# Kernel tuning notes

Hardware: AMD Instinct MI355X
Metric: run time of the kernel (lower is better)

The kernel has to match this reference:

```python
import jax, jax.numpy as jnp
from jax import lax
import numpy as np

B, N, D_MODEL = 4, 2048, 768
D_INNER = 1536      # int(2.0 * d_model)
DT_RANK = 48        # ceil(768 / 16)
EPS = 1e-5


def setup_inputs() -> dict:
    key = jax.random.key(0)
    ks = jax.random.split(key, 9)
    x = jax.random.normal(ks[0], (B, N, D_MODEL), jnp.float32)
    # BFS order: a permutation of node ids
    sorted_index = jax.random.permutation(ks[1], N).astype(jnp.int32)
    # parent BFS position of node at BFS position i, must be < i; root (i=0) has -1
    pos = jnp.arange(N)
    r = jax.random.randint(ks[2], (N,), 0, N)
    sorted_parent = jnp.where(pos == 0, -1, r % jnp.maximum(pos, 1)).astype(jnp.int32)
    s = 0.02
    in_proj_w = jax.random.normal(ks[3], (D_MODEL, 2 * D_INNER), jnp.float32) * s
    x_proj_w = jax.random.normal(ks[4], (D_INNER, DT_RANK + 2), jnp.float32) * s
    dt_proj_w = jax.random.normal(ks[5], (DT_RANK, D_INNER), jnp.float32) * (DT_RANK ** -0.5)
    # dt bias init: softplus^{-1}(dt) with dt ~ LogUniform(1e-3, 1e-1)
    dt = jnp.exp(jax.random.uniform(ks[6], (D_INNER,)) * (np.log(0.1) - np.log(0.001)) + np.log(0.001))
    dt_proj_b = (dt + jnp.log(-jnp.expm1(-dt))).astype(jnp.float32)
    A_log = jnp.zeros((D_INNER,), jnp.float32)   # log(A=1) per original init (d_state=1)
    D_param = jnp.ones((D_INNER,), jnp.float32)
    ln_gamma = jnp.ones((D_INNER,), jnp.float32)
    ln_beta = jnp.zeros((D_INNER,), jnp.float32)
    out_proj_w = jax.random.normal(ks[7], (D_INNER, D_MODEL), jnp.float32) * s
    return dict(x=x, sorted_index=sorted_index, sorted_parent=sorted_parent,
                in_proj_w=in_proj_w, x_proj_w=x_proj_w, dt_proj_w=dt_proj_w,
                dt_proj_b=dt_proj_b, A_log=A_log, D_param=D_param,
                ln_gamma=ln_gamma, ln_beta=ln_beta, out_proj_w=out_proj_w)


def _tree_ssm_recurrence(dBx, dA, sorted_index, sorted_parent):
    """h[bfs i] = dA[node(i)] * h[parent_bfs(i)] + dBx[node(i)]. Inputs (B,N,Di) node-major."""
    b, n, di = dBx.shape
    dA_bfs = jnp.take(dA, sorted_index, axis=1)    # (B,N,Di) in BFS order
    dBx_bfs = jnp.take(dBx, sorted_index, axis=1)

    def step(h_buf, inp):
        t, par, dA_t, dBx_t = inp                   # dA_t/dBx_t: (B,Di)
        h_par = h_buf[:, jnp.maximum(par, 0)]       # (B,Di) gather at parent BFS pos
        h_par = jnp.where(par < 0, jnp.zeros_like(h_par), h_par)
        h_t = dA_t * h_par + dBx_t
        return h_buf.at[:, t].set(h_t), h_t

    xs = (jnp.arange(n), sorted_parent,
          dA_bfs.transpose(1, 0, 2), dBx_bfs.transpose(1, 0, 2))
    _, h_bfs = lax.scan(step, jnp.zeros((b, n, di), dBx.dtype), xs)
    # scatter BFS-order states back to node-id order
    h = jnp.zeros((b, n, di), dBx.dtype).at[:, sorted_index].set(h_bfs.transpose(1, 0, 2))
    return h


def reference(x, sorted_index, sorted_parent, in_proj_w, x_proj_w, dt_proj_w,
              dt_proj_b, A_log, D_param, ln_gamma, ln_beta, out_proj_w):
    xz = x @ in_proj_w                              # (B,N,2*Di)
    x_inner, z = jnp.split(xz, 2, axis=-1)
    z = jax.nn.silu(z)
    x_dbl = x_inner @ x_proj_w                      # (B,N,dt_rank+2)
    dt_lr, B_ssm, C_ssm = (x_dbl[..., :DT_RANK], x_dbl[..., DT_RANK:DT_RANK + 1],
                           x_dbl[..., DT_RANK + 1:DT_RANK + 2])
    dt = jax.nn.softplus(dt_lr @ dt_proj_w + dt_proj_b)  # (B,N,Di)
    As = -jnp.exp(A_log)                            # (Di,) negative
    dA = jnp.exp(dt * As)                           # (B,N,Di) in (0,1)
    dBx = dt * B_ssm * x_inner                      # (B,N,Di)
    h = _tree_ssm_recurrence(dBx, dA, sorted_index, sorted_parent)
    y = h * C_ssm + D_param * x_inner               # (B,N,Di)
    mu = jnp.mean(y, axis=-1, keepdims=True)
    var = jnp.mean(jnp.square(y - mu), axis=-1, keepdims=True)
    y = (y - mu) * lax.rsqrt(var + EPS) * ln_gamma + ln_beta
    y = y * z
    return y @ out_proj_w                           # (B,N,D)
```

## Files before the change

kernel.cpp:

```cpp
#include <hip/hip_runtime.h>
#include <math.h>


#define ROWS 8192
#define DIN 1536
#define DMOD 768
#define NSEQ 2048
#define DTR 48
#define NSPLIT 4

typedef __bf16 bfrag __attribute__((ext_vector_type(8)));
typedef float f4 __attribute__((ext_vector_type(4)));

__device__ __forceinline__ unsigned short f2bf(float f) {
  unsigned int u = __float_as_uint(f);
  unsigned int r = (u + 0x7fffu + ((u >> 16) & 1u)) >> 16;
  return (unsigned short)r;
}
__device__ __forceinline__ float bf2f(unsigned short h) {
  return __uint_as_float(((unsigned int)h) << 16);
}

__device__ __forceinline__ void gld_lds16(const void* g, void* l) {
  __builtin_amdgcn_global_load_lds((const __attribute__((address_space(1))) void*)g,
                                   (__attribute__((address_space(3))) void*)l, 16, 0, 0);
}

__device__ __forceinline__ void barx() {
  asm volatile("" ::: "memory");
  __builtin_amdgcn_s_barrier();
  asm volatile("" ::: "memory");
}

template <int MODE, int NCOLS>
__global__ __launch_bounds__(512, 2) void gemm_dp(
    const unsigned short* __restrict__ A, const unsigned short* __restrict__ Bt,
    void* __restrict__ C0v, void* __restrict__ C1v, int K, int ldc) {
  __shared__ unsigned short lds[2][(128 + 192) * 64];
  const int tid = threadIdx.x;
  const int w = tid >> 6, l = tid & 63;
  const int quad = l >> 4, l16 = l & 15;
  const int wr = w >> 2, wc = w & 3;
  const int h = blockIdx.x + gridDim.x * blockIdx.y;
  const int chunk = (gridDim.x * gridDim.y) >> 3;
  const int swz = (h & 7) * chunk + (h >> 3);
  const int row0 = (swz / NCOLS) * 128, col0 = (swz % NCOLS) * 192;
  const int nt = K >> 6;

  const int srow = tid >> 3;
  const int schunk = ((tid & 7) ^ (srow & 7)) * 8;
  const unsigned short* aS = A + (size_t)(row0 + srow) * K + schunk;
  const unsigned short* bS = Bt + (size_t)(col0 + srow) * K + schunk;

#define STG_A(bufi, q, kt)                                     \
  gld_lds16(aS + (size_t)((q) * 64) * K + (size_t)(kt) * 64,   \
            (char*)&lds[bufi][(q) * 4096] + w * 1024)
#define STG_B(bufi, q, kt)                                     \
  gld_lds16(bS + (size_t)((q) * 64) * K + (size_t)(kt) * 64,   \
            (char*)&lds[bufi][8192 + (q) * 4096] + w * 1024)

  const int arow = (wr * 64 + l16) * 64;
  const int brow = (wc * 48 + l16) * 64;
  int cs[2];
  cs[0] = (quad ^ (l16 & 7)) * 8;
  cs[1] = ((4 + quad) ^ (l16 & 7)) * 8;

#define RDA(m, ks) (*(const bfrag*)(const void*)(LA + arow + (m) * 1024 + cs[ks]))
#define RDB(n, ks) (*(const bfrag*)(const void*)(LB + brow + (n) * 1024 + cs[ks]))

  f4 acc[4][3];
#pragma unroll
  for (int m = 0; m < 4; m++)
#pragma unroll
    for (int n = 0; n < 3; n++) acc[m][n] = (f4){0.f, 0.f, 0.f, 0.f};

  const int kt1 = (nt > 1) ? 1 : 0;
#pragma unroll
  for (int q = 0; q < 2; q++) STG_A(0, q, 0);
#pragma unroll
  for (int q = 0; q < 3; q++) STG_B(0, q, 0);
#pragma unroll
  for (int q = 0; q < 2; q++) STG_A(1, q, kt1);
#pragma unroll
  for (int q = 0; q < 3; q++) STG_B(1, q, kt1);
  asm volatile("s_waitcnt vmcnt(5)" ::: "memory");
  barx();

  for (int t = 0; t < nt; ++t) {
    const int b = t & 1;
    const unsigned short* LA = &lds[b][0];
    const unsigned short* LB = &lds[b][8192];
    const int kA = (t + 2 < nt) ? (t + 2) : (nt - 1);
    bfrag af[4][2], bfr[3][2];

#pragma unroll
    for (int m = 0; m < 4; m++) {
      af[m][0] = RDA(m, 0);
      af[m][1] = RDA(m, 1);
    }
#pragma unroll
    for (int n = 0; n < 3; n++) {
      bfr[n][0] = RDB(n, 0);
      bfr[n][1] = RDB(n, 1);
    }
    asm volatile("s_waitcnt lgkmcnt(0)" ::: "memory");
    barx();
    STG_A(b, 0, kA);
    STG_A(b, 1, kA);
    STG_B(b, 0, kA);
    STG_B(b, 1, kA);
    STG_B(b, 2, kA);
    __builtin_amdgcn_s_setprio(1);
#pragma unroll
    for (int m = 0; m < 4; m++)
#pragma unroll
      for (int n = 0; n < 3; n++) {
        acc[m][n] = __builtin_amdgcn_mfma_f32_16x16x32_bf16(af[m][0], bfr[n][0], acc[m][n], 0, 0, 0);
        acc[m][n] = __builtin_amdgcn_mfma_f32_16x16x32_bf16(af[m][1], bfr[n][1], acc[m][n], 0, 0, 0);
      }
    __builtin_amdgcn_s_setprio(0);
    asm volatile("s_waitcnt vmcnt(5)" ::: "memory");
    barx();
  }
  asm volatile("s_waitcnt vmcnt(0)" ::: "memory");

#undef STG_A
#undef STG_B
#undef RDA
#undef RDB

  if (MODE == 0) {
    float* C0 = (float*)C0v;
    const int cb = col0 + wc * 48 + l16;
#pragma unroll
    for (int m = 0; m < 4; m++) {
      const int rb = row0 + wr * 64 + m * 16 + quad * 4;
#pragma unroll
      for (int n = 0; n < 3; n++)
#pragma unroll
        for (int r = 0; r < 4; r++)
          C0[(size_t)(rb + r) * ldc + cb + n * 16] = acc[m][n][r];
    }
  } else {
    const bool is_z = (col0 >= DIN);
    unsigned short* dst = is_z ? (unsigned short*)C1v : (unsigned short*)C0v;
    const int cb = col0 + wc * 48 + l16 - (is_z ? DIN : 0);
#pragma unroll
    for (int m = 0; m < 4; m++) {
      const int rb = row0 + wr * 64 + m * 16 + quad * 4;
#pragma unroll
      for (int n = 0; n < 3; n++)
#pragma unroll
        for (int r = 0; r < 4; r++) {
          float v = acc[m][n][r];
          if (is_z) v = v / (1.f + __expf(-v));
          dst[(size_t)(rb + r) * DIN + cb + n * 16] = f2bf(v);
        }
    }
  }
}

__global__ __launch_bounds__(1024) void prep1_kernel(
    const int* __restrict__ sidx, const int* __restrict__ spar,
    int* __restrict__ SLOT_PACK, int* __restrict__ SLOTINV,
    int* __restrict__ LSTART, int* __restrict__ NLEV,
    const float* __restrict__ x, unsigned short* __restrict__ Xbf,
    const float* __restrict__ xpw, unsigned short* __restrict__ XPW,
    const float* __restrict__ dtw, unsigned short* __restrict__ DTWb,
    const float* __restrict__ A_log, float* __restrict__ negA) {
  const int bi = blockIdx.x;
  const int tid = threadIdx.x;
  if (bi == 0) {
    __shared__ int par[2048], idx[2048], ancA[2048], ancB[2048], rnkA[2048], rnkB[2048];
    __shared__ int dmax;
    for (int i = tid; i < 2048; i += 1024) {
      const int p = spar[i];
      par[i] = p;
      idx[i] = sidx[i];
      ancA[i] = (p < 0) ? -1 : p;
      rnkA[i] = (p < 0) ? 0 : 1;
    }
    if (tid == 0) dmax = 0;
    __syncthreads();
    for (int r = 0; r < 11; r++) {
      int* ca = (r & 1) ? ancB : ancA;
      int* cr = (r & 1) ? rnkB : rnkA;
      int* na = (r & 1) ? ancA : ancB;
      int* nr = (r & 1) ? rnkA : rnkB;
      for (int i = tid; i < 2048; i += 1024) {
        const int a = ca[i], rv = cr[i];
        if (a >= 0) {
          nr[i] = rv + cr[a];
          na[i] = ca[a];
        } else {
          nr[i] = rv;
          na[i] = a;
        }
      }
      __syncthreads();
    }
    for (int i = tid; i < 2048; i += 1024) ancA[i] = 0;
    __syncthreads();
    for (int i = tid; i < 2048; i += 1024) {
      atomicAdd(&ancA[rnkB[i]], 1);
      atomicMax(&dmax, rnkB[i]);
    }
    __syncthreads();
    for (int s = 0; s < 11; s++) {
      const int off = 1 << s;
      int* cur = (s & 1) ? ancB : ancA;
      int* nxt = (s & 1) ? ancA : ancB;
      for (int i = tid; i < 2048; i += 1024) {
        int v = cur[i];
        if (i >= off) v += cur[i - off];
        nxt[i] = v;
      }
      __syncthreads();
    }
    for (int i = tid; i < 2049; i += 1024) {
      const int v = (i == 0) ? 0 : ancB[i - 1];
      LSTART[i] = v;
      if (i < 2048) rnkA[i] = v;
    }
    if (tid == 0) NLEV[0] = dmax + 1;
    __syncthreads();
    for (int i = tid; i < 2048; i += 1024) {
      const int d = rnkB[i];
      const int slot = atomicAdd(&rnkA[d], 1);
      const int node = idx[i];
      const int p = par[i];
      const int pn = (p < 0) ? -1 : idx[p];
      SLOT_PACK[slot] = node | ((pn + 1) << 12);
      SLOTINV[node] = slot;
    }
  } else if (bi < 1 + 1536) {
    const int i = ((bi - 1) * 1024 + tid) * 4;
    const float4 v = *(const float4*)(x + i);
    union { unsigned short h[4]; uint2 u; } pk;
    pk.h[0] = f2bf(v.x);
    pk.h[1] = f2bf(v.y);
    pk.h[2] = f2bf(v.z);
    pk.h[3] = f2bf(v.w);
    *(uint2*)(Xbf + i) = pk.u;
  } else if (bi < 1 + 1536 + 96) {
    const int i = (bi - 1537) * 1024 + tid;
    const int c = i / 1536, k = i % 1536;
    XPW[i] = (c < 50) ? f2bf(xpw[(size_t)k * 50 + c]) : (unsigned short)0;
  } else if (bi < 1 + 1536 + 96 + 96) {
    const int i = (bi - 1633) * 1024 + tid;
    const int d = i >> 6, k = i & 63;
    DTWb[i] = (k < 48) ? f2bf(dtw[(size_t)k * DIN + d]) : (unsigned short)0;
  } else {
    const int i = (bi - 1729) * 1024 + tid;
    if (i < DIN) negA[i] = -__expf(A_log[i]);
  }
}

__global__ __launch_bounds__(256) void prep2_kernel(
    const float* __restrict__ W1, unsigned short* __restrict__ W1t,
    const float* __restrict__ W2, unsigned short* __restrict__ W2t) {
  __shared__ float t[32][33];
  int idx = blockIdx.x;
  const float* W;
  unsigned short* Wt;
  int K, N, n0, k0;
  if (idx < 2304) {
    W = W1; Wt = W1t; K = DMOD; N = 2 * DIN;
    n0 = (idx % 96) * 32; k0 = (idx / 96) * 32;
  } else {
    idx -= 2304;
    W = W2; Wt = W2t; K = DIN; N = DMOD;
    n0 = (idx % 24) * 32; k0 = (idx / 24) * 32;
  }
  const int tx = threadIdx.x & 31, ty = threadIdx.x >> 5;
  for (int i = ty; i < 32; i += 8) t[i][tx] = W[(size_t)(k0 + i) * N + n0 + tx];
  __syncthreads();
  for (int i = ty; i < 32; i += 8)
    Wt[(size_t)(n0 + i) * K + k0 + tx] = f2bf(t[tx][i]);
}

__global__ __launch_bounds__(256) void xdbl_mfma(
    const unsigned short* __restrict__ XI, const unsigned short* __restrict__ XPW,
    float* __restrict__ XP) {
  __shared__ unsigned short As[128 * 32];
  __shared__ unsigned short Bs[64 * 32];
  const int tid = threadIdx.x;
  const int w = tid >> 6, l = tid & 63;
  const int quad = l >> 4, l16 = l & 15;
  const int h = blockIdx.x + 4 * blockIdx.y;
  const int swz = (h & 7) * 32 + (h >> 3);
  const int split = swz & 3;
  const int row0 = (swz >> 2) * 128;
  const int kbase = split * (DIN / NSPLIT);

  f4 acc[2][4];
#pragma unroll
  for (int i = 0; i < 2; i++)
#pragma unroll
    for (int j = 0; j < 4; j++) acc[i][j] = (f4){0.f, 0.f, 0.f, 0.f};

  const int srow = w * 16 + (l >> 2);
  const int kcol = (((l & 3) ^ ((l >> 2) & 3)) * 8);
  const int qs = (quad ^ (l16 & 3)) * 8;

  for (int c = 0; c < 12; c++) {
    const int k0 = kbase + c * 32;
#pragma unroll
    for (int r = 0; r < 2; r++) {
      gld_lds16(XI + (size_t)(row0 + srow + r * 64) * DIN + k0 + kcol,
                (char*)As + r * 4096 + w * 1024);
    }
    gld_lds16(XPW + (size_t)srow * DIN + k0 + kcol, (char*)Bs + w * 1024);
    __syncthreads();
    bfrag af[2], bf[4];
#pragma unroll
    for (int i = 0; i < 2; i++)
      af[i] = *(const bfrag*)(const void*)(As + (w * 32 + i * 16 + l16) * 32 + qs);
#pragma unroll
    for (int j = 0; j < 4; j++)
      bf[j] = *(const bfrag*)(const void*)(Bs + (j * 16 + l16) * 32 + qs);
#pragma unroll
    for (int i = 0; i < 2; i++)
#pragma unroll
      for (int j = 0; j < 4; j++)
        acc[i][j] = __builtin_amdgcn_mfma_f32_16x16x32_bf16(af[i], bf[j], acc[i][j], 0, 0, 0);
    __syncthreads();
  }

  float* dst = XP + (size_t)split * ROWS * 64 + (size_t)row0 * 64;
#pragma unroll
  for (int i = 0; i < 2; i++) {
    const int rb = w * 32 + i * 16 + quad * 4;
#pragma unroll
    for (int j = 0; j < 4; j++) {
      const int col = j * 16 + l16;
#pragma unroll
      for (int r = 0; r < 4; r++) dst[(size_t)(rb + r) * 64 + col] = acc[i][j][r];
    }
  }
}

__global__ __launch_bounds__(256) void xp_reduce(
    const float* __restrict__ XP, unsigned short* __restrict__ DTLRb,
    float* __restrict__ BCv, float* __restrict__ CCv) {
  const int i = blockIdx.x * 256 + threadIdx.x;
  const int row = i >> 4, c4 = (i & 15) * 4;
  const float* p = XP + (size_t)row * 64 + c4;
  float4 s = make_float4(0.f, 0.f, 0.f, 0.f);
#pragma unroll
  for (int sp = 0; sp < NSPLIT; sp++) {
    const float4 v = *(const float4*)(p + (size_t)sp * ROWS * 64);
    s.x += v.x;
    s.y += v.y;
    s.z += v.z;
    s.w += v.w;
  }
  if (c4 == 48) {
    BCv[row] = s.x;
    CCv[row] = s.y;
  }
  union { unsigned short h[4]; uint2 u; } pk;
  pk.h[0] = f2bf(s.x);
  pk.h[1] = f2bf(s.y);
  pk.h[2] = f2bf(s.z);
  pk.h[3] = f2bf(s.w);
  *(uint2*)(DTLRb + (size_t)row * 64 + c4) = pk.u;
}

__global__ __launch_bounds__(256) void dt_gemm(
    const unsigned short* __restrict__ DTLRb, const unsigned short* __restrict__ DTWb,
    const float* __restrict__ bias, const float* __restrict__ negA,
    const float* __restrict__ BCv, const unsigned short* __restrict__ XI,
    const int* __restrict__ SLOTINV,
    unsigned short* __restrict__ DAp, unsigned short* __restrict__ DBXp) {
  __shared__ unsigned short As[2][64 * 32];
  __shared__ unsigned short Bs[2][128 * 32];
  __shared__ int sinv[64];
  __shared__ float bcs[64];
  const int tid = threadIdx.x;
  const int w = tid >> 6, l = tid & 63;
  const int quad = l >> 4, l16 = l & 15;
  const int wrow = (w >> 1) * 32, wcol = (w & 1) * 64;
  const int h = blockIdx.x + 12 * blockIdx.y;
  const int swz = (h & 7) * 192 + (h >> 3);
  const int row0 = (swz / 12) * 64, col0 = (swz % 12) * 128;
  const int p0 = row0 & (NSEQ - 1);
  const int bbase = row0 & ~(NSEQ - 1);
  const int srow = w * 16 + (l >> 2);
  const int koff = (((l & 3) ^ ((l >> 2) & 3)) * 8);
  const int qs = (quad ^ (l16 & 3)) * 8;

#pragma unroll
  for (int c = 0; c < 2; c++) {
    gld_lds16(DTLRb + (size_t)(row0 + srow) * 64 + c * 32 + koff,
              (char*)As[c] + w * 1024);
#pragma unroll
    for (int r = 0; r < 2; r++)
      gld_lds16(DTWb + (size_t)(col0 + srow + r * 64) * 64 + c * 32 + koff,
                (char*)Bs[c] + r * 4096 + w * 1024);
  }
  if (tid < 64) {
    sinv[tid] = SLOTINV[p0 + tid];
    bcs[tid] = BCv[row0 + tid];
  }
  __syncthreads();

  f4 acc[2][4];
#pragma unroll
  for (int i = 0; i < 2; i++)
#pragma unroll
    for (int j = 0; j < 4; j++) acc[i][j] = (f4){0.f, 0.f, 0.f, 0.f};

#pragma unroll
  for (int c = 0; c < 2; c++) {
    bfrag af[2], bf[4];
#pragma unroll
    for (int i = 0; i < 2; i++)
      af[i] = *(const bfrag*)(const void*)(As[c] + (wrow + i * 16 + l16) * 32 + qs);
#pragma unroll
    for (int j = 0; j < 4; j++)
      bf[j] = *(const bfrag*)(const void*)(Bs[c] + (wcol + j * 16 + l16) * 32 + qs);
#pragma unroll
    for (int i = 0; i < 2; i++)
#pragma unroll
      for (int j = 0; j < 4; j++)
        acc[i][j] = __builtin_amdgcn_mfma_f32_16x16x32_bf16(af[i], bf[j], acc[i][j], 0, 0, 0);
  }

  float bj[4], aj[4];
#pragma unroll
  for (int j = 0; j < 4; j++) {
    const int d = col0 + wcol + j * 16 + l16;
    bj[j] = bias[d];
    aj[j] = negA[d];
  }
#pragma unroll
  for (int i = 0; i < 2; i++) {
#pragma unroll
    for (int r = 0; r < 4; r++) {
      const int row_l = wrow + i * 16 + quad * 4 + r;
      const int row = row0 + row_l;
      const float bc = bcs[row_l];
      const size_t rp = (size_t)(bbase + sinv[row_l]) * DIN;
#pragma unroll
      for (int j = 0; j < 4; j++) {
        const int d = col0 + wcol + j * 16 + l16;
        const float s = acc[i][j][r] + bj[j];
        const float sp = fmaxf(s, 0.f) + __logf(1.f + __expf(-fabsf(s)));
        const float xi = bf2f(XI[(size_t)row * DIN + d]);
        DAp[rp + d] = f2bf(__expf(sp * aj[j]));
        DBXp[rp + d] = f2bf(sp * bc * xi);
      }
    }
  }
}

__global__ __launch_bounds__(256) void recur_kernel(
    const unsigned short* __restrict__ DAp, const unsigned short* __restrict__ DBXp,
    unsigned short* __restrict__ Hb,
    const int* __restrict__ SLOT_PACK, const int* __restrict__ LSTART,
    const int* __restrict__ NLEV) {
  __shared__ unsigned short hl[NSEQ * 16];
  __shared__ int spack[NSEQ];
  __shared__ int lst[258];
  const int tid = threadIdx.x;
  const int bid = blockIdx.x;
  const int logical = (bid & 7) * 48 + (bid >> 3);
  const int c8a = logical * 2;
  const int b = c8a / 192;
  const int d8a = c8a % 192;
  const int nlev = NLEV[0];
  for (int i = tid; i < NSEQ; i += 256) spack[i] = SLOT_PACK[i];
  const int nl = (nlev + 1 < 258) ? nlev + 1 : 258;
  for (int i = tid; i < nl; i += 256) lst[i] = LSTART[i];
  __syncthreads();

  for (int L = 0; L < nlev; L++) {
    const int s0 = (L < 257) ? lst[L] : LSTART[L];
    const int s1 = (L + 1 < 258) ? lst[L + 1] : LSTART[L + 1];
    const int items = (s1 - s0) * 2;
    for (int it = tid; it < items; it += 256) {
      const int s = s0 + (it >> 1);
      const int ch = it & 1;
      const size_t goff = (size_t)(b * NSEQ + s) * DIN + (d8a + ch) * 8;
      union { uint4 u; unsigned short h[8]; } da, dbx, hpu, hvu;
      da.u = *(const uint4*)(DAp + goff);
      dbx.u = *(const uint4*)(DBXp + goff);
      const int pk = spack[s];
      const int node = pk & 4095;
      const int pn = (pk >> 12) - 1;
      float hp[8];
      if (pn >= 0) {
        hpu.u = *(const uint4*)(hl + pn * 16 + ch * 8);
#pragma unroll
        for (int e = 0; e < 8; e++) hp[e] = bf2f(hpu.h[e]);
      } else {
#pragma unroll
        for (int e = 0; e < 8; e++) hp[e] = 0.f;
      }
#pragma unroll
      for (int e = 0; e < 8; e++) {
        const float hv = fmaf(bf2f(da.h[e]), hp[e], bf2f(dbx.h[e]));
        hvu.h[e] = f2bf(hv);
      }
      *(uint4*)(hl + node * 16 + ch * 8) = hvu.u;
    }
    __syncthreads();
  }

  for (int i = tid; i < NSEQ * 2; i += 256) {
    const int node = i >> 1, ch = i & 1;
    *(uint4*)(Hb + (size_t)(b * NSEQ + node) * DIN + (d8a + ch) * 8) =
        *(const uint4*)(hl + node * 16 + ch * 8);
  }
}

__global__ __launch_bounds__(192) void ln_kernel(
    const unsigned short* __restrict__ Hb, const float* __restrict__ CCv,
    const unsigned short* __restrict__ XI, const float* __restrict__ Dp,
    const float* __restrict__ gamma, const float* __restrict__ beta,
    const unsigned short* __restrict__ Z, unsigned short* __restrict__ YLN) {
  const int row = blockIdx.x;
  const int tid = threadIdx.x;
  const int d8 = tid * 8;
  const float C = CCv[row];
  const size_t base = (size_t)row * DIN + d8;
  union U { uint4 u; unsigned short h[8]; };
  U hu, xu;
  hu.u = *(const uint4*)(Hb + base);
  xu.u = *(const uint4*)(XI + base);
  float dp[8];
  *(float4*)(dp) = *(const float4*)(Dp + d8);
  *(float4*)(dp + 4) = *(const float4*)(Dp + d8 + 4);
  float y[8];
  float s = 0.f, s2 = 0.f;
#pragma unroll
  for (int e = 0; e < 8; e++) {
    const float v = fmaf(bf2f(hu.h[e]), C, dp[e] * bf2f(xu.h[e]));
    y[e] = v;
    s += v;
    s2 = fmaf(v, v, s2);
  }
#pragma unroll
  for (int off = 32; off >= 1; off >>= 1) {
    s += __shfl_down(s, off);
    s2 += __shfl_down(s2, off);
  }
  __shared__ float rs[3], rs2[3];
  const int w = tid >> 6;
  if ((tid & 63) == 0) {
    rs[w] = s;
    rs2[w] = s2;
  }
  __syncthreads();
  const float ts = rs[0] + rs[1] + rs[2];
  const float ts2 = rs2[0] + rs2[1] + rs2[2];
  const float mu = ts * (1.f / 1536.f);
  const float var = ts2 * (1.f / 1536.f) - mu * mu;
  const float inv = rsqrtf(var + 1e-5f);
  float g[8], bb[8];
  *(float4*)(g) = *(const float4*)(gamma + d8);
  *(float4*)(g + 4) = *(const float4*)(gamma + d8 + 4);
  *(float4*)(bb) = *(const float4*)(beta + d8);
  *(float4*)(bb + 4) = *(const float4*)(beta + d8 + 4);
  U zu, out;
  zu.u = *(const uint4*)(Z + base);
#pragma unroll
  for (int e = 0; e < 8; e++) {
    const float o = (y[e] - mu) * inv * g[e] + bb[e];
    out.h[e] = f2bf(o * bf2f(zu.h[e]));
  }
  *(uint4*)(YLN + base) = out.u;
}

extern "C" void kernel_launch(void* const* d_in, const int* in_sizes, int n_in,
                              void* d_out, int out_size, void* d_ws, size_t ws_size,
                              hipStream_t stream) {
  const float* x = (const float*)d_in[0];
  const int* sidx = (const int*)d_in[1];
  const int* spar = (const int*)d_in[2];
  const float* in_proj = (const float*)d_in[3];
  const float* x_proj = (const float*)d_in[4];
  const float* dt_proj = (const float*)d_in[5];
  const float* dt_b = (const float*)d_in[6];
  const float* A_log = (const float*)d_in[7];
  const float* Dp = (const float*)d_in[8];
  const float* gamma = (const float*)d_in[9];
  const float* beta = (const float*)d_in[10];
  const float* out_proj = (const float*)d_in[11];
  float* out = (float*)d_out;

  char* p = (char*)d_ws;
  const size_t RC = (size_t)ROWS * DIN;
  unsigned short* XI = (unsigned short*)p;   p += RC * 2;
  unsigned short* Z = (unsigned short*)p;    p += RC * 2;
  unsigned short* DAp = (unsigned short*)p;  p += RC * 2;
  unsigned short* DBXp = (unsigned short*)p; p += RC * 2;
  unsigned short* Hb = (unsigned short*)p;   p += RC * 2;
  float* XP = (float*)p;                     p += (size_t)NSPLIT * ROWS * 64 * 4;
  unsigned short* DTLRb = (unsigned short*)p; p += (size_t)ROWS * 64 * 2;
  float* BCv = (float*)p;                    p += ROWS * 4;
  float* CCv = (float*)p;                    p += ROWS * 4;
  float* negA = (float*)p;                   p += DIN * 4;
  unsigned short* Xbf = (unsigned short*)p;  p += (size_t)ROWS * DMOD * 2;
  unsigned short* W1t = (unsigned short*)p;  p += (size_t)2 * DIN * DMOD * 2;
  unsigned short* W2t = (unsigned short*)p;  p += (size_t)DMOD * DIN * 2;
  unsigned short* XPW = (unsigned short*)p;  p += (size_t)64 * DIN * 2;
  unsigned short* DTWb = (unsigned short*)p; p += (size_t)DIN * 64 * 2;
  int* ipart = (int*)p;
  int* SLOT_PACK = ipart;
  int* SLOTINV = ipart + 2048;
  int* LSTART = ipart + 4096;
  int* NLEV = ipart + 4096 + 2049;
  unsigned short* YLN = DAp;

  prep1_kernel<<<1731, 1024, 0, stream>>>(sidx, spar, SLOT_PACK, SLOTINV,
                                          LSTART, NLEV, x, Xbf, x_proj, XPW,
                                          dt_proj, DTWb, A_log, negA);
  prep2_kernel<<<3456, 256, 0, stream>>>(in_proj, W1t, out_proj, W2t);
  gemm_dp<1, 16><<<dim3(16, 64), 512, 0, stream>>>(Xbf, W1t, XI, Z, DMOD, 0);
  xdbl_mfma<<<dim3(NSPLIT, 64), 256, 0, stream>>>(XI, XPW, XP);
  xp_reduce<<<ROWS * 16 / 256, 256, 0, stream>>>(XP, DTLRb, BCv, CCv);
  dt_gemm<<<dim3(12, 128), 256, 0, stream>>>(DTLRb, DTWb, dt_b, negA, BCv, XI,
                                             SLOTINV, DAp, DBXp);
  recur_kernel<<<384, 256, 0, stream>>>(DAp, DBXp, Hb, SLOT_PACK, LSTART, NLEV);
  ln_kernel<<<ROWS, 192, 0, stream>>>(Hb, CCv, XI, Dp, gamma, beta, Z, YLN);
  gemm_dp<0, 4><<<dim3(4, 64), 512, 0, stream>>>(YLN, W2t, out, nullptr, DIN, DMOD);
}
```

Measured before the change: 267.2 us.

## Fold x_proj into in_proj weights to compute x_dbl directly from input

Precomputes a combined weight in_proj[:, :Di] @ x_proj (768x50) in a new prep kernel. x_dbl is then computed directly from the bf16 input with K=768 instead of from x_inner with K=1536. This removes the split-K partial buffer, the reduction kernel, and the dependency on the big in_proj GEMM. The trade-offs are an extra per-call weight-product kernel and a change in rounding, since x_inner is no longer rounded to bf16 before the projection.

```diff
diff --git a/kernel.cpp b/kernel.cpp
--- a/kernel.cpp
+++ b/kernel.cpp
@@ -7,7 +7,6 @@
 #define DMOD 768
 #define NSEQ 2048
 #define DTR 48
-#define NSPLIT 4
 
 typedef __bf16 bfrag __attribute__((ext_vector_type(8)));
 typedef float f4 __attribute__((ext_vector_type(4)));
@@ -165,7 +164,6 @@
     int* __restrict__ SLOT_PACK, int* __restrict__ SLOTINV,
     int* __restrict__ LSTART, int* __restrict__ NLEV,
     const float* __restrict__ x, unsigned short* __restrict__ Xbf,
-    const float* __restrict__ xpw, unsigned short* __restrict__ XPW,
     const float* __restrict__ dtw, unsigned short* __restrict__ DTWb,
     const float* __restrict__ A_log, float* __restrict__ negA) {
   const int bi = blockIdx.x;
@@ -244,14 +242,10 @@
     *(uint2*)(Xbf + i) = pk.u;
   } else if (bi < 1 + 1536 + 96) {
     const int i = (bi - 1537) * 1024 + tid;
-    const int c = i / 1536, k = i % 1536;
-    XPW[i] = (c < 50) ? f2bf(xpw[(size_t)k * 50 + c]) : (unsigned short)0;
-  } else if (bi < 1 + 1536 + 96 + 96) {
-    const int i = (bi - 1633) * 1024 + tid;
     const int d = i >> 6, k = i & 63;
     DTWb[i] = (k < 48) ? f2bf(dtw[(size_t)k * DIN + d]) : (unsigned short)0;
   } else {
-    const int i = (bi - 1729) * 1024 + tid;
+    const int i = (bi - 1633) * 1024 + tid;
     if (i < DIN) negA[i] = -__expf(A_log[i]);
   }
 }
@@ -279,92 +273,88 @@
     Wt[(size_t)(n0 + i) * K + k0 + tx] = f2bf(t[tx][i]);
 }
 
-__global__ __launch_bounds__(256) void xdbl_mfma(
-    const unsigned short* __restrict__ XI, const unsigned short* __restrict__ XPW,
-    float* __restrict__ XP) {
-  __shared__ unsigned short As[128 * 32];
+__global__ __launch_bounds__(256) void cwprep_kernel(
+    const float* __restrict__ W1, const float* __restrict__ xpw,
+    unsigned short* __restrict__ CWt) {
+  const int tid = threadIdx.x;
+  const int kk = tid >> 6, lane = tid & 63;
+  const int k = blockIdx.x * 4 + kk;
+  float acc[50];
+#pragma unroll
+  for (int c = 0; c < 50; c++) acc[c] = 0.f;
+  const float* wrow = W1 + (size_t)k * (2 * DIN);
+  for (int j = lane; j < DIN; j += 64) {
+    const float wv = wrow[j];
+    const float* xr = xpw + (size_t)j * 50;
+#pragma unroll
+    for (int c = 0; c < 50; c++) acc[c] = fmaf(wv, xr[c], acc[c]);
+  }
+#pragma unroll
+  for (int c = 0; c < 50; c++) {
+#pragma unroll
+    for (int off = 32; off >= 1; off >>= 1) acc[c] += __shfl_down(acc[c], off);
+  }
+  if (lane == 0) {
+#pragma unroll
+    for (int c = 0; c < 50; c++) CWt[(size_t)c * DMOD + k] = f2bf(acc[c]);
+  }
+  if (tid < 56) {
+    const int c = 50 + (tid >> 2);
+    const int kz = blockIdx.x * 4 + (tid & 3);
+    CWt[(size_t)c * DMOD + kz] = 0;
+  }
+}
+
+__global__ __launch_bounds__(256) void xdbl2_mfma(
+    const unsigned short* __restrict__ Xbf, const unsigned short* __restrict__ CWt,
+    unsigned short* __restrict__ DTLRb, float* __restrict__ BCv,
+    float* __restrict__ CCv) {
+  __shared__ unsigned short As[64 * 32];
   __shared__ unsigned short Bs[64 * 32];
   const int tid = threadIdx.x;
   const int w = tid >> 6, l = tid & 63;
   const int quad = l >> 4, l16 = l & 15;
-  const int h = blockIdx.x + 4 * blockIdx.y;
-  const int swz = (h & 7) * 32 + (h >> 3);
-  const int split = swz & 3;
-  const int row0 = (swz >> 2) * 128;
-  const int kbase = split * (DIN / NSPLIT);
-
-  f4 acc[2][4];
-#pragma unroll
-  for (int i = 0; i < 2; i++)
-#pragma unroll
-    for (int j = 0; j < 4; j++) acc[i][j] = (f4){0.f, 0.f, 0.f, 0.f};
+  const int h = blockIdx.x;
+  const int swz = (h & 7) * 16 + (h >> 3);
+  const int row0 = swz * 64;
+
+  f4 acc[4];
+#pragma unroll
+  for (int j = 0; j < 4; j++) acc[j] = (f4){0.f, 0.f, 0.f, 0.f};
 
   const int srow = w * 16 + (l >> 2);
   const int kcol = (((l & 3) ^ ((l >> 2) & 3)) * 8);
   const int qs = (quad ^ (l16 & 3)) * 8;
 
-  for (int c = 0; c < 12; c++) {
-    const int k0 = kbase + c * 32;
-#pragma unroll
-    for (int r = 0; r < 2; r++) {
-      gld_lds16(XI + (size_t)(row0 + srow + r * 64) * DIN + k0 + kcol,
-                (char*)As + r * 4096 + w * 1024);
-    }
-    gld_lds16(XPW + (size_t)srow * DIN + k0 + kcol, (char*)Bs + w * 1024);
+  for (int c = 0; c < 24; c++) {
+    const int k0 = c * 32;
+    gld_lds16(Xbf + (size_t)(row0 + srow) * DMOD + k0 + kcol,
+              (char*)As + w * 1024);
+    gld_lds16(CWt + (size_t)srow * DMOD + k0 + kcol, (char*)Bs + w * 1024);
     __syncthreads();
-    bfrag af[2], bf[4];
-#pragma unroll
-    for (int i = 0; i < 2; i++)
-      af[i] = *(const bfrag*)(const void*)(As + (w * 32 + i * 16 + l16) * 32 + qs);
+    bfrag af, bf[4];
+    af = *(const bfrag*)(const void*)(As + (w * 16 + l16) * 32 + qs);
 #pragma unroll
     for (int j = 0; j < 4; j++)
       bf[j] = *(const bfrag*)(const void*)(Bs + (j * 16 + l16) * 32 + qs);
 #pragma unroll
-    for (int i = 0; i < 2; i++)
-#pragma unroll
-      for (int j = 0; j < 4; j++)
-        acc[i][j] = __builtin_amdgcn_mfma_f32_16x16x32_bf16(af[i], bf[j], acc[i][j], 0, 0, 0);
+    for (int j = 0; j < 4; j++)
+      acc[j] = __builtin_amdgcn_mfma_f32_16x16x32_bf16(af, bf[j], acc[j], 0, 0, 0);
     __syncthreads();
   }
 
-  float* dst = XP + (size_t)split * ROWS * 64 + (size_t)row0 * 64;
-#pragma unroll
-  for (int i = 0; i < 2; i++) {
-    const int rb = w * 32 + i * 16 + quad * 4;
-#pragma unroll
-    for (int j = 0; j < 4; j++) {
-      const int col = j * 16 + l16;
-#pragma unroll
-      for (int r = 0; r < 4; r++) dst[(size_t)(rb + r) * 64 + col] = acc[i][j][r];
-    }
-  }
-}
-
-__global__ __launch_bounds__(256) void xp_reduce(
-    const float* __restrict__ XP, unsigned short* __restrict__ DTLRb,
-    float* __restrict__ BCv, float* __restrict__ CCv) {
-  const int i = blockIdx.x * 256 + threadIdx.x;
-  const int row = i >> 4, c4 = (i & 15) * 4;
-  const float* p = XP + (size_t)row * 64 + c4;
-  float4 s = make_float4(0.f, 0.f, 0.f, 0.f);
-#pragma unroll
-  for (int sp = 0; sp < NSPLIT; sp++) {
-    const float4 v = *(const float4*)(p + (size_t)sp * ROWS * 64);
-    s.x += v.x;
-    s.y += v.y;
-    s.z += v.z;
-    s.w += v.w;
-  }
-  if (c4 == 48) {
-    BCv[row] = s.x;
-    CCv[row] = s.y;
-  }
-  union { unsigned short h[4]; uint2 u; } pk;
-  pk.h[0] = f2bf(s.x);
-  pk.h[1] = f2bf(s.y);
-  pk.h[2] = f2bf(s.z);
-  pk.h[3] = f2bf(s.w);
-  *(uint2*)(DTLRb + (size_t)row * 64 + c4) = pk.u;
+#pragma unroll
+  for (int j = 0; j < 4; j++) {
+    const int col = j * 16 + l16;
+#pragma unroll
+    for (int r = 0; r < 4; r++) {
+      const int row = row0 + w * 16 + quad * 4 + r;
+      const float v = acc[j][r];
+      DTLRb[(size_t)row * 64 + col] = f2bf(v);
+      if (col == 48) BCv[row] = v;
+      else if (col == 49) CCv[row] = v;
+    }
+  }
 }
 
 __global__ __launch_bounds__(256) void dt_gemm(
@@ -597,7 +587,6 @@
   unsigned short* DAp = (unsigned short*)p;  p += RC * 2;
   unsigned short* DBXp = (unsigned short*)p; p += RC * 2;
   unsigned short* Hb = (unsigned short*)p;   p += RC * 2;
-  float* XP = (float*)p;                     p += (size_t)NSPLIT * ROWS * 64 * 4;
   unsigned short* DTLRb = (unsigned short*)p; p += (size_t)ROWS * 64 * 2;
   float* BCv = (float*)p;                    p += ROWS * 4;
   float* CCv = (float*)p;                    p += ROWS * 4;
@@ -605,7 +594,7 @@
   unsigned short* Xbf = (unsigned short*)p;  p += (size_t)ROWS * DMOD * 2;
   unsigned short* W1t = (unsigned short*)p;  p += (size_t)2 * DIN * DMOD * 2;
   unsigned short* W2t = (unsigned short*)p;  p += (size_t)DMOD * DIN * 2;
-  unsigned short* XPW = (unsigned short*)p;  p += (size_t)64 * DIN * 2;
+  unsigned short* CWt = (unsigned short*)p;  p += (size_t)64 * DMOD * 2;
   unsigned short* DTWb = (unsigned short*)p; p += (size_t)DIN * 64 * 2;
   int* ipart = (int*)p;
   int* SLOT_PACK = ipart;
@@ -614,13 +603,13 @@
   int* NLEV = ipart + 4096 + 2049;
   unsigned short* YLN = DAp;
 
-  prep1_kernel<<<1731, 1024, 0, stream>>>(sidx, spar, SLOT_PACK, SLOTINV,
-                                          LSTART, NLEV, x, Xbf, x_proj, XPW,
-                                          dt_proj, DTWb, A_log, negA);
+  prep1_kernel<<<1635, 1024, 0, stream>>>(sidx, spar, SLOT_PACK, SLOTINV,
+                                          LSTART, NLEV, x, Xbf, dt_proj, DTWb,
+                                          A_log, negA);
   prep2_kernel<<<3456, 256, 0, stream>>>(in_proj, W1t, out_proj, W2t);
+  cwprep_kernel<<<192, 256, 0, stream>>>(in_proj, x_proj, CWt);
+  xdbl2_mfma<<<128, 256, 0, stream>>>(Xbf, CWt, DTLRb, BCv, CCv);
   gemm_dp<1, 16><<<dim3(16, 64), 512, 0, stream>>>(Xbf, W1t, XI, Z, DMOD, 0);
-  xdbl_mfma<<<dim3(NSPLIT, 64), 256, 0, stream>>>(XI, XPW, XP);
-  xp_reduce<<<ROWS * 16 / 256, 256, 0, stream>>>(XP, DTLRb, BCv, CCv);
   dt_gemm<<<dim3(12, 128), 256, 0, stream>>>(DTLRb, DTWb, dt_b, negA, BCv, XI,
                                              SLOTINV, DAp, DBXp);
   recur_kernel<<<384, 256, 0, stream>>>(DAp, DBXp, Hb, SLOT_PACK, LSTART, NLEV);
```

Measured after the change: 284.8 us. 6.6% more time.
